# Performance work log

Hardware: AMD Instinct MI355X
Metric: run time of the kernel (lower is better)

The kernel has to match this reference:

```python
import jax, jax.numpy as jnp
import numpy as np

B, OUT, IN, G = 256, 256, 256, 8


def setup_inputs() -> dict:
    key = jax.random.key(0)
    k1, k2, k3, k4 = jax.random.split(key, 4)
    x = jax.random.normal(k1, (B, IN), dtype=jnp.float32)
    # xavier-like scale for spline_weight
    spline_weight = jax.random.normal(k2, (OUT, IN, G), dtype=jnp.float32) * 0.06
    # scaler initialized to ones in torch; use positive values near 1 to exercise the exp
    spline_scaler = jax.random.uniform(k3, (OUT, IN), dtype=jnp.float32, minval=0.5, maxval=1.5)
    # base_activation initialized to zeros in torch; small random to exercise the residual path
    base_activation = jax.random.normal(k4, (OUT, IN), dtype=jnp.float32) * 0.02
    grid = jnp.linspace(-2.0, 2.0, G, dtype=jnp.float32)
    return {
        "x": x,
        "spline_weight": spline_weight,
        "spline_scaler": spline_scaler,
        "base_activation": base_activation,
        "grid": grid,
    }


def reference(x, spline_weight, spline_scaler, base_activation, grid):
    # x: (B, IN) -> out: (B, OUT)
    xn = jnp.tanh(x)                                        # (B, IN)
    # RBF-like basis: exp(-|tanh(x) - grid| * scaler), shape (B, OUT, IN, G)
    dist = jnp.abs(xn[:, None, :, None] - grid[None, None, None, :])  # (B, 1, IN, G)
    basis = jnp.exp(-dist * spline_scaler[None, :, :, None])          # (B, OUT, IN, G)
    # reduce over grid dim with the spline weights
    spline_out = jnp.einsum('boig,oig->boi', basis, spline_weight)    # (B, OUT, IN)
    out = spline_out + base_activation[None, :, :] * xn[:, None, :]   # (B, OUT, IN)
    return jnp.sum(out, axis=-1)                                      # (B, OUT)
```

## Files before the change

### kernel.cpp

```cpp
#include <hip/hip_runtime.h>


#define B_   256
#define OUT_ 256
#define IN_  256
#define G_   8
#define NK   5
#define SCH  32
#define BT   8
#define ICH  (IN_/SCH)

__global__ void kan_prep(const float* __restrict__ x,
                         const float* __restrict__ w,
                         const float* __restrict__ sc,
                         const float* __restrict__ ba,
                         const float* __restrict__ grid,
                         float2* __restrict__ xnk,
                         float2* __restrict__ sbt,
                         float2* __restrict__ T)
{
    const int idx = blockIdx.x * 256 + threadIdx.x;

    float g[G_];
#pragma unroll
    for (int j = 0; j < G_; ++j) g[j] = grid[j];

    {
        const float xv = x[idx];
        const float xn = tanhf(xv);
        int k = 0;
#pragma unroll
        for (int j = 0; j < G_; ++j) k += (g[j] <= xn) ? 1 : 0;
        k = min(max(k, 2), 6) - 2;
        const int row = k * IN_ + (idx & 255);
        xnk[idx] = make_float2(xn, __int_as_float(row));
    }

    {
        const int o = idx >> 8;
        const int i = idx & 255;
        const int base = o * IN_ + i;
        const float s  = sc[base];
        const float bv = ba[base];

        float Ep[G_], Em[G_];
#pragma unroll
        for (int j = 0; j < G_; ++j) {
            const float wv = w[base * G_ + j];
            const float t  = s * g[j];
            Ep[j] = wv * expf(t);
            Em[j] = wv * expf(-t);
        }
#pragma unroll
        for (int kk = 0; kk < NK; ++kk) {
            const int k = kk + 2;
            float A = 0.f, Bv = 0.f;
#pragma unroll
            for (int j = 0; j < G_; ++j) {
                if (j < k) A += Ep[j]; else Bv += Em[j];
            }
            T[(kk * IN_ + i) * OUT_ + o] = make_float2(A, Bv);
        }
        sbt[i * OUT_ + o] = make_float2(s * 1.44269504088896340736f, bv);
    }
}

__global__ __launch_bounds__(256, 4) void kan_main(
        const float2* __restrict__ xnk,
        const float2* __restrict__ sbt,
        const float2* __restrict__ T,
        float* __restrict__ partial)
{
    const int o    = threadIdx.x;
    const int bgrp = blockIdx.x & 31;
    const int ic   = blockIdx.x >> 5;
    const int b0   = bgrp * BT;
    const int i0   = ic * ICH;

    __shared__ float2 sxnk[BT][ICH];
    if (threadIdx.x < BT * ICH) {
        const int bb = threadIdx.x / ICH;
        const int ii = threadIdx.x % ICH;
        sxnk[bb][ii] = xnk[(b0 + bb) * IN_ + i0 + ii];
    }
    __syncthreads();

    float acc[BT];
#pragma unroll
    for (int j = 0; j < BT; ++j) acc[j] = 0.f;

    for (int ii = 0; ii < ICH; ++ii) {
        const int i = i0 + ii;
        const float2 sb = sbt[i * OUT_ + o];
#pragma unroll
        for (int bb = 0; bb < BT; ++bb) {
            const float2 xk = sxnk[bb][ii];
            const float xn  = xk.x;
            const int   row = __float_as_int(xk.y);
            const float2 rec = T[(row << 8) + o];
            const float t = sb.x * xn;
            const float P = exp2f(-t);
            const float M = exp2f(t);
            float a = fmaf(sb.y, xn, acc[bb]);
            a       = fmaf(P, rec.x, a);
            acc[bb] = fmaf(M, rec.y, a);
        }
    }

    float* pout = partial + (size_t)ic * (B_ * OUT_) + b0 * OUT_ + o;
#pragma unroll
    for (int bb = 0; bb < BT; ++bb) pout[bb * OUT_] = acc[bb];
}

__global__ void kan_reduce(const float* __restrict__ partial,
                           float* __restrict__ out)
{
    const int idx = blockIdx.x * 256 + threadIdx.x;
    float s = 0.f;
#pragma unroll
    for (int c = 0; c < SCH; ++c) s += partial[c * (B_ * OUT_) + idx];
    out[idx] = s;
}

extern "C" void kernel_launch(void* const* d_in, const int* in_sizes, int n_in,
                              void* d_out, int out_size, void* d_ws, size_t ws_size,
                              hipStream_t stream)
{
    const float* x    = (const float*)d_in[0];
    const float* w    = (const float*)d_in[1];
    const float* sc   = (const float*)d_in[2];
    const float* ba   = (const float*)d_in[3];
    const float* grid = (const float*)d_in[4];
    float* out = (float*)d_out;

    char* ws = (char*)d_ws;
    float2* xnk = (float2*)(ws);
    float2* sbt = (float2*)(ws + 512 * 1024);
    float2* T   = (float2*)(ws + 1024 * 1024);
    float*  partial = (float*)(ws + 1024 * 1024 + (size_t)NK * IN_ * OUT_ * sizeof(float2));

    kan_prep<<<(B_ * IN_) / 256, 256, 0, stream>>>(x, w, sc, ba, grid, xnk, sbt, T);
    kan_main<<<SCH * (B_ / BT), 256, 0, stream>>>(xnk, sbt, T, partial);
    kan_reduce<<<(B_ * OUT_) / 256, 256, 0, stream>>>(partial, out);
}
```

Before: 87.01 us.

## Replace split-IN partials and reduce kernel with in-block shared-memory reduction

```diff
diff --git a/kernel.cpp b/kernel.cpp
--- a/kernel.cpp
+++ b/kernel.cpp
@@ -6,9 +6,8 @@
 #define IN_  256
 #define G_   8
 #define NK   5
-#define SCH  32
-#define BT   8
-#define ICH  (IN_/SCH)
+#define BT   2
+#define OT   64
 
 __global__ void kan_prep(const float* __restrict__ x,
                          const float* __restrict__ w,
@@ -19,26 +18,24 @@
                          float2* __restrict__ sbt,
                          float2* __restrict__ T)
 {
-    const int idx = blockIdx.x * 256 + threadIdx.x;
-
     float g[G_];
 #pragma unroll
     for (int j = 0; j < G_; ++j) g[j] = grid[j];
 
     {
-        const float xv = x[idx];
-        const float xn = tanhf(xv);
+        const int idx = blockIdx.x * 256 + threadIdx.x;
+        const float xn = tanhf(x[idx]);
         int k = 0;
 #pragma unroll
         for (int j = 0; j < G_; ++j) k += (g[j] <= xn) ? 1 : 0;
         k = min(max(k, 2), 6) - 2;
-        const int row = k * IN_ + (idx & 255);
+        const int row = k * IN_ + (idx & (IN_ - 1));
         xnk[idx] = make_float2(xn, __int_as_float(row));
     }
 
     {
-        const int o = idx >> 8;
-        const int i = idx & 255;
+        const int i = blockIdx.x;
+        const int o = threadIdx.x;
         const int base = o * IN_ + i;
         const float s  = sc[base];
         const float bv = ba[base];
@@ -48,8 +45,8 @@
         for (int j = 0; j < G_; ++j) {
             const float wv = w[base * G_ + j];
             const float t  = s * g[j];
-            Ep[j] = wv * expf(t);
-            Em[j] = wv * expf(-t);
+            Ep[j] = wv * __expf(t);
+            Em[j] = wv * __expf(-t);
         }
 #pragma unroll
         for (int kk = 0; kk < NK; ++kk) {
@@ -65,61 +62,58 @@
     }
 }
 
-__global__ __launch_bounds__(256, 4) void kan_main(
+__global__ __launch_bounds__(256, 8) void kan_main(
         const float2* __restrict__ xnk,
         const float2* __restrict__ sbt,
         const float2* __restrict__ T,
-        float* __restrict__ partial)
+        float* __restrict__ out)
 {
-    const int o    = threadIdx.x;
-    const int bgrp = blockIdx.x & 31;
-    const int ic   = blockIdx.x >> 5;
-    const int b0   = bgrp * BT;
-    const int i0   = ic * ICH;
+    const int lane = threadIdx.x & 63;
+    const int igrp = threadIdx.x >> 6;
+    const int ot   = blockIdx.x & 3;
+    const int bg   = blockIdx.x >> 2;
+    const int o    = ot * OT + lane;
+    const int b0   = bg * BT;
 
-    __shared__ float2 sxnk[BT][ICH];
-    if (threadIdx.x < BT * ICH) {
-        const int bb = threadIdx.x / ICH;
-        const int ii = threadIdx.x % ICH;
-        sxnk[bb][ii] = xnk[(b0 + bb) * IN_ + i0 + ii];
-    }
+    __shared__ float2 sxk[BT * IN_];
+    __shared__ float  sacc[4][BT][OT];
+
+    for (int t = threadIdx.x; t < BT * IN_; t += 256)
+        sxk[t] = xnk[b0 * IN_ + t];
     __syncthreads();
 
     float acc[BT];
 #pragma unroll
-    for (int j = 0; j < BT; ++j) acc[j] = 0.f;
+    for (int bb = 0; bb < BT; ++bb) acc[bb] = 0.f;
 
-    for (int ii = 0; ii < ICH; ++ii) {
+    const int i0 = igrp * 64;
+    for (int ii = 0; ii < 64; ++ii) {
         const int i = i0 + ii;
         const float2 sb = sbt[i * OUT_ + o];
 #pragma unroll
         for (int bb = 0; bb < BT; ++bb) {
-            const float2 xk = sxnk[bb][ii];
+            const float2 xk = sxk[bb * IN_ + i];
             const float xn  = xk.x;
             const int   row = __float_as_int(xk.y);
             const float2 rec = T[(row << 8) + o];
             const float t = sb.x * xn;
-            const float P = exp2f(-t);
-            const float M = exp2f(t);
             float a = fmaf(sb.y, xn, acc[bb]);
-            a       = fmaf(P, rec.x, a);
-            acc[bb] = fmaf(M, rec.y, a);
+            a       = fmaf(exp2f(-t), rec.x, a);
+            acc[bb] = fmaf(exp2f(t),  rec.y, a);
         }
     }
 
-    float* pout = partial + (size_t)ic * (B_ * OUT_) + b0 * OUT_ + o;
 #pragma unroll
-    for (int bb = 0; bb < BT; ++bb) pout[bb * OUT_] = acc[bb];
-}
+    for (int bb = 0; bb < BT; ++bb) sacc[igrp][bb][lane] = acc[bb];
+    __syncthreads();
 
-__global__ void kan_reduce(const float* __restrict__ partial,
-                           float* __restrict__ out)
-{
-    const int idx = blockIdx.x * 256 + threadIdx.x;
-    float s = 0.f;
-#pragma unroll
-    for (int c = 0; c < SCH; ++c) s += partial[c * (B_ * OUT_) + idx];
-    out[idx] = s;
+    if (threadIdx.x < BT * OT) {
+        const int bb = threadIdx.x >> 6;
+        const int l  = threadIdx.x & 63;
+        const float s = sacc[0][bb][l] + sacc[1][bb][l]
+                      + sacc[2][bb][l] + sacc[3][bb][l];
+        out[(b0 + bb) * OUT_ + ot * OT + l] = s;
+    }
 }
 
 extern "C" void kernel_launch(void* const* d_in, const int* in_sizes, int n_in,
@@ -137,9 +131,7 @@
     float2* xnk = (float2*)(ws);
     float2* sbt = (float2*)(ws + 512 * 1024);
     float2* T   = (float2*)(ws + 1024 * 1024);
-    float*  partial = (float*)(ws + 1024 * 1024 + (size_t)NK * IN_ * OUT_ * sizeof(float2));
 
-    kan_prep<<<(B_ * IN_) / 256, 256, 0, stream>>>(x, w, sc, ba, grid, xnk, sbt, T);
-    kan_main<<<SCH * (B_ / BT), 256, 0, stream>>>(xnk, sbt, T, partial);
-    kan_reduce<<<(B_ * OUT_) / 256, 256, 0, stream>>>(partial, out);
+    kan_prep<<<IN_, 256, 0, stream>>>(x, w, sc, ba, grid, xnk, sbt, T);
+    kan_main<<<(B_ / BT) * (OUT_ / OT), 256, 0, stream>>>(xnk, sbt, T, out);
 }
```

Result: faster. 83.67 us (-3.8%).
